# Kernel optimization log

Measured on AMD Instinct MI355X. Metric: run time of the kernel, lower is better.

## Reference

```python
import jax, jax.numpy as jnp
import numpy as np

B, H, T = 16, 2048, 512


def setup_inputs() -> dict:
    key = jax.random.key(0)
    ks = jax.random.split(key, 9)
    s = 1.0 / np.sqrt(H)
    return {
        "traj_z": jax.random.normal(ks[0], (B, H), dtype=jnp.float32),
        "traj_input": jax.random.normal(ks[1], (B, T), dtype=jnp.float32),
        "w_ih": jax.random.uniform(ks[2], (3 * H, 1), jnp.float32, -s, s),
        "b_ih": jax.random.uniform(ks[3], (3 * H,), jnp.float32, -s, s),
        "w_hh": jax.random.uniform(ks[4], (3 * H, H), jnp.float32, -s, s),
        "b_hh": jax.random.uniform(ks[5], (3 * H,), jnp.float32, -s, s),
        "w_traj": jax.random.uniform(ks[6], (1, H), jnp.float32, -s, s),
        "b_traj": jax.random.uniform(ks[7], (1,), jnp.float32, -s, s),
        "timesteps": T,
    }


def reference(traj_z, traj_input, w_ih, b_ih, w_hh, b_hh, w_traj, b_traj, timesteps):
    # epoch = inf -> teacher-forcing mask is all zeros -> blend is identity.
    x0 = traj_input[:, 0:1]  # [B, 1]

    def step(carry, _):
        h, x = carry
        gi = x @ w_ih.T + b_ih            # [B, 3H]
        gh = h @ w_hh.T + b_hh            # [B, 3H]
        i_r, i_z, i_n = jnp.split(gi, 3, axis=-1)
        h_r, h_z, h_n = jnp.split(gh, 3, axis=-1)
        r = jax.nn.sigmoid(i_r + h_r)
        z = jax.nn.sigmoid(i_z + h_z)
        n = jnp.tanh(i_n + r * h_n)
        h_new = (1.0 - z) * n + z * h     # GRUCell update
        x_new = h_new @ w_traj.T + b_traj + x  # residual linear head, [B, 1]
        return (h_new, x_new), x_new

    _, ys = jax.lax.scan(step, (traj_z, x0), None, length=timesteps)
    return jnp.transpose(ys, (1, 0, 2))  # [B, T, 1]
```

## Files before the change

kernel.cpp:

```cpp
#include <hip/hip_runtime.h>
#include <stdint.h>
#include <math.h>

#define Hdim   2048
#define Bdim   16
#define Tsteps 512
#define NWG    128
#define TPB    256
#define KC     16
#define NCHUNK 16
#define FLAGSTRIDE 32
#define HBYTES (Bdim * Hdim * 2)

typedef __attribute__((ext_vector_type(8))) short short8_t;
typedef __attribute__((ext_vector_type(4))) float f32x4;
typedef __attribute__((ext_vector_type(4))) unsigned int u32x4;

__device__ __forceinline__ short f2bf(float x) {
  uint32_t u = __builtin_bit_cast(uint32_t, x);
  u += 0x7fffu + ((u >> 16) & 1u);
  return (short)(u >> 16);
}

__device__ __forceinline__ short8_t load8_bf(const float* __restrict__ p) {
  short8_t r;
#pragma unroll
  for (int j = 0; j < 8; ++j) r[j] = f2bf(p[j]);
  return r;
}

__device__ __forceinline__ void publish(uint32_t* flags, int wg, int tid, uint32_t n) {
  asm volatile("s_waitcnt vmcnt(0)" ::: "memory");
  __syncthreads();
  if (tid == 0)
    __hip_atomic_store(flags + wg * FLAGSTRIDE, n, __ATOMIC_RELAXED, __HIP_MEMORY_SCOPE_AGENT);
}
__device__ __forceinline__ void waitall(const uint32_t* flags, int tid, uint32_t n) {
  if (tid < NWG) {
    while (__hip_atomic_load(flags + tid * FLAGSTRIDE, __ATOMIC_RELAXED,
                             __HIP_MEMORY_SCOPE_AGENT) < n) {
      __builtin_amdgcn_s_sleep(1);
    }
  }
  __syncthreads();
}


__device__ __forceinline__ void publish_h(uint32_t* hbuf32, int buf,
                                          int eb, int ekc, int ecol, float h_own) {
  uint32_t mybits = (uint32_t)(uint16_t)f2bf(h_own);
  uint32_t n1 = (uint32_t)__shfl_xor((int)mybits, 1, 64);
  uint32_t a  = (mybits & 0xffffu) | (n1 << 16);
  uint32_t b  = (uint32_t)__shfl_xor((int)a, 2, 64);
  uint32_t c4 = (uint32_t)__shfl_xor((int)a, 4, 64);
  uint32_t d  = (uint32_t)__shfl_xor((int)b, 4, 64);
  if ((ekc & 7) == 0) {
    u32x4 q; q.x = a; q.y = b; q.z = c4; q.w = d;
    char* dst = (char*)hbuf32 + (size_t)buf * HBYTES
              + ((size_t)(ecol >> 3) * 256 + (size_t)eb * 16);
    asm volatile("global_store_dwordx4 %0, %1, off sc0 sc1" :: "v"(dst), "v"(q) : "memory");
  }
}

__global__ void __launch_bounds__(TPB, 1) traj_kernel(
    const float* __restrict__ traj_z, const float* __restrict__ traj_input,
    const float* __restrict__ w_ih, const float* __restrict__ b_ih,
    const float* __restrict__ w_hh, const float* __restrict__ b_hh,
    const float* __restrict__ w_traj, const float* __restrict__ b_traj,
    float* __restrict__ out, uint32_t* __restrict__ hbuf32, uint32_t* __restrict__ flags)
{
  const int tid  = threadIdx.x;
  const int wg   = blockIdx.x;
  const int wave = tid >> 6;
  const int lane = tid & 63;
  const int ln16 = lane & 15;
  const int quad = lane >> 4;
  const int colbase = wg * KC;
  const int kwave   = wave * (Hdim / 4);

  __shared__ float s_red[4][3][16][16];
  __shared__ float s_x3[4][16];

  short8_t wf0[NCHUNK], wf1[NCHUNK], wf2[NCHUNK], wt[NCHUNK];
#pragma unroll
  for (int c = 0; c < NCHUNK; ++c) {
    const int k0 = kwave + c * 32 + quad * 8;
    wf0[c] = load8_bf(w_hh + (size_t)(0 * Hdim + colbase + ln16) * Hdim + k0);
    wf1[c] = load8_bf(w_hh + (size_t)(1 * Hdim + colbase + ln16) * Hdim + k0);
    wf2[c] = load8_bf(w_hh + (size_t)(2 * Hdim + colbase + ln16) * Hdim + k0);
    short8_t g = {0, 0, 0, 0, 0, 0, 0, 0};
    if (ln16 == 0) g = load8_bf(w_traj + k0);
    wt[c] = g;
  }

  const int eb   = tid >> 4;
  const int ekc  = tid & 15;
  const int ecol = colbase + ekc;
  const float wr = w_ih[ecol], wz = w_ih[Hdim + ecol], wn = w_ih[2 * Hdim + ecol];
  const float br = b_ih[ecol] + b_hh[ecol];
  const float bz = b_ih[Hdim + ecol] + b_hh[Hdim + ecol];
  const float bin = b_ih[2 * Hdim + ecol];
  const float bhn = b_hh[2 * Hdim + ecol];
  const float bt  = b_traj[0];
  float h_own = traj_z[eb * Hdim + ecol];
  float x_reg = traj_input[eb * Tsteps];

  publish_h(hbuf32, 0, eb, ekc, ecol, h_own);
  publish(flags, wg, tid, 1);

  for (int i = 0; i <= Tsteps; ++i) {
    waitall(flags, tid, (uint32_t)(i + 1));

    const char* hbase = (const char*)hbuf32 + (size_t)(i & 1) * HBYTES
                      + (size_t)(kwave >> 5) * 1024 + (size_t)lane * 16;
    short8_t af[NCHUNK];
#pragma unroll
    for (int c = 0; c < NCHUNK; ++c) {
      short8_t t;
      asm volatile("global_load_dwordx4 %0, %1, off sc0 sc1"
                   : "=v"(t) : "v"(hbase + (size_t)c * 1024));
      af[c] = t;
    }
    asm volatile("s_waitcnt vmcnt(0)" ::: "memory");
    __builtin_amdgcn_sched_barrier(0);

    f32x4 a0 = {0.f, 0.f, 0.f, 0.f}, a1 = a0, a2 = a0, a3 = a0;
#pragma unroll
    for (int c = 0; c < NCHUNK; ++c) {
      a0 = __builtin_amdgcn_mfma_f32_16x16x32_bf16(af[c], wf0[c], a0, 0, 0, 0);
      a1 = __builtin_amdgcn_mfma_f32_16x16x32_bf16(af[c], wf1[c], a1, 0, 0, 0);
      a2 = __builtin_amdgcn_mfma_f32_16x16x32_bf16(af[c], wf2[c], a2, 0, 0, 0);
      a3 = __builtin_amdgcn_mfma_f32_16x16x32_bf16(af[c], wt[c],  a3, 0, 0, 0);
    }

#pragma unroll
    for (int r = 0; r < 4; ++r) {
      const int m = quad * 4 + r;
      s_red[wave][0][m][ln16] = a0[r];
      s_red[wave][1][m][ln16] = a1[r];
      s_red[wave][2][m][ln16] = a2[r];
    }
    if (ln16 == 0) {
#pragma unroll
      for (int r = 0; r < 4; ++r) s_x3[wave][quad * 4 + r] = a3[r];
    }
    __syncthreads();

    if (i > 0) {
      const float xd = ((s_x3[0][eb] + s_x3[1][eb]) + s_x3[2][eb]) + s_x3[3][eb];
      x_reg += xd + bt;
      if (wg == 0 && ekc == 0) out[eb * Tsteps + (i - 1)] = x_reg;
    }
    if (i == Tsteps) break;

    const float gr = ((s_red[0][0][eb][ekc] + s_red[1][0][eb][ekc]) + s_red[2][0][eb][ekc]) + s_red[3][0][eb][ekc];
    const float gz = ((s_red[0][1][eb][ekc] + s_red[1][1][eb][ekc]) + s_red[2][1][eb][ekc]) + s_red[3][1][eb][ekc];
    const float gn = ((s_red[0][2][eb][ekc] + s_red[1][2][eb][ekc]) + s_red[2][2][eb][ekc]) + s_red[3][2][eb][ekc];
    const float x  = x_reg;
    const float rr = 1.f / (1.f + expf(-(x * wr + br + gr)));
    const float zz = 1.f / (1.f + expf(-(x * wz + bz + gz)));
    const float nn = tanhf(x * wn + bin + rr * (gn + bhn));
    h_own = (1.f - zz) * nn + zz * h_own;

    publish_h(hbuf32, (i + 1) & 1, eb, ekc, ecol, h_own);
    publish(flags, wg, tid, (uint32_t)(i + 2));
  }
}

extern "C" void kernel_launch(void* const* d_in, const int* in_sizes, int n_in,
                              void* d_out, int out_size, void* d_ws, size_t ws_size,
                              hipStream_t stream) {
  const float* traj_z     = (const float*)d_in[0];
  const float* traj_input = (const float*)d_in[1];
  const float* w_ih   = (const float*)d_in[2];
  const float* b_ih   = (const float*)d_in[3];
  const float* w_hh   = (const float*)d_in[4];
  const float* b_hh   = (const float*)d_in[5];
  const float* w_traj = (const float*)d_in[6];
  const float* b_traj = (const float*)d_in[7];
  float* out = (float*)d_out;

  uint8_t*  ws    = (uint8_t*)d_ws;
  uint32_t* flags = (uint32_t*)ws;
  uint32_t* hbuf  = (uint32_t*)(ws + NWG * FLAGSTRIDE * 4);

  (void)hipMemsetAsync(flags, 0, NWG * FLAGSTRIDE * 4, stream);
  hipLaunchKernelGGL(traj_kernel, dim3(NWG), dim3(TPB), 0, stream,
                     traj_z, traj_input, w_ih, b_ih, w_hh, b_hh, w_traj, b_traj,
                     out, hbuf, flags);
}
```

Measured before the change: 1.907 ms.

## Halve workgroup count with two column tiles each and publish partial head dots

The persistent kernel now runs 64 workgroups, each owning 32 hidden columns instead of 16. Five gate weight fragments stay in registers and the sixth (n gate, second tile) lives in LDS. The trajectory head is no longer an extra MFMA. Each workgroup publishes a partial dot product of its new h columns with w_traj, and every workgroup sums all 64 partials after the barrier. This is meant to halve the number of participants in the per-step grid barrier and drop the wasted head MFMA, at the cost of more MFMA and LDS work per workgroup and an extra global load per step.

```diff
diff --git a/kernel.cpp b/kernel.cpp
--- a/kernel.cpp
+++ b/kernel.cpp
@@ -5,9 +5,9 @@
 #define Hdim   2048
 #define Bdim   16
 #define Tsteps 512
-#define NWG    128
+#define NWG    64
 #define TPB    256
-#define KC     16
+#define KC     32
 #define NCHUNK 16
 #define FLAGSTRIDE 32
 #define HBYTES (Bdim * Hdim * 2)
@@ -44,7 +44,6 @@
   }
   __syncthreads();
 }
-
 
 __device__ __forceinline__ void publish_h(uint32_t* hbuf32, int buf,
                                           int eb, int ekc, int ecol, float h_own) {
@@ -62,12 +61,27 @@
   }
 }
 
+__device__ __forceinline__ void publish_part(float* partbuf, int buf, int wg,
+                                             int eb, int ekc,
+                                             float h0, float w0, float h1, float w1) {
+  float pd = h0 * w0 + h1 * w1;
+  pd += __shfl_xor(pd, 1, 64);
+  pd += __shfl_xor(pd, 2, 64);
+  pd += __shfl_xor(pd, 4, 64);
+  pd += __shfl_xor(pd, 8, 64);
+  if (ekc == 0) {
+    float* dst = partbuf + (size_t)buf * (Bdim * 64) + (size_t)eb * 64 + wg;
+    asm volatile("global_store_dword %0, %1, off sc0 sc1" :: "v"(dst), "v"(pd) : "memory");
+  }
+}
+
 __global__ void __launch_bounds__(TPB, 1) traj_kernel(
     const float* __restrict__ traj_z, const float* __restrict__ traj_input,
     const float* __restrict__ w_ih, const float* __restrict__ b_ih,
     const float* __restrict__ w_hh, const float* __restrict__ b_hh,
     const float* __restrict__ w_traj, const float* __restrict__ b_traj,
-    float* __restrict__ out, uint32_t* __restrict__ hbuf32, uint32_t* __restrict__ flags)
+    float* __restrict__ out, uint32_t* __restrict__ hbuf32,
+    float* __restrict__ partbuf, uint32_t* __restrict__ flags)
 {
   const int tid  = threadIdx.x;
   const int wg   = blockIdx.x;
@@ -77,35 +91,52 @@
   const int quad = lane >> 4;
   const int colbase = wg * KC;
   const int kwave   = wave * (Hdim / 4);
-
-  __shared__ float s_red[4][3][16][16];
-  __shared__ float s_x3[4][16];
-
-  short8_t wf0[NCHUNK], wf1[NCHUNK], wf2[NCHUNK], wt[NCHUNK];
+  const int gcbase  = wave * NCHUNK;
+
+  __shared__ short8_t s_wn1[64][64];
+  __shared__ float s_red[4][3][2][16][16];
+
+  for (int idx = tid; idx < 64 * 64; idx += TPB) {
+    const int gc = idx >> 6, l = idx & 63;
+    const int col = colbase + 16 + (l & 15);
+    const int k0  = gc * 32 + (l >> 4) * 8;
+    s_wn1[gc][l] = load8_bf(w_hh + (size_t)(2 * Hdim + col) * Hdim + k0);
+  }
+
+  short8_t fr0[NCHUNK], fz0[NCHUNK], fn0[NCHUNK], fr1[NCHUNK], fz1[NCHUNK];
 #pragma unroll
   for (int c = 0; c < NCHUNK; ++c) {
     const int k0 = kwave + c * 32 + quad * 8;
-    wf0[c] = load8_bf(w_hh + (size_t)(0 * Hdim + colbase + ln16) * Hdim + k0);
-    wf1[c] = load8_bf(w_hh + (size_t)(1 * Hdim + colbase + ln16) * Hdim + k0);
-    wf2[c] = load8_bf(w_hh + (size_t)(2 * Hdim + colbase + ln16) * Hdim + k0);
-    short8_t g = {0, 0, 0, 0, 0, 0, 0, 0};
-    if (ln16 == 0) g = load8_bf(w_traj + k0);
-    wt[c] = g;
+    fr0[c] = load8_bf(w_hh + (size_t)(0 * Hdim + colbase + ln16) * Hdim + k0);
+    fz0[c] = load8_bf(w_hh + (size_t)(1 * Hdim + colbase + ln16) * Hdim + k0);
+    fn0[c] = load8_bf(w_hh + (size_t)(2 * Hdim + colbase + ln16) * Hdim + k0);
+    fr1[c] = load8_bf(w_hh + (size_t)(0 * Hdim + colbase + 16 + ln16) * Hdim + k0);
+    fz1[c] = load8_bf(w_hh + (size_t)(1 * Hdim + colbase + 16 + ln16) * Hdim + k0);
   }
 
   const int eb   = tid >> 4;
   const int ekc  = tid & 15;
-  const int ecol = colbase + ekc;
-  const float wr = w_ih[ecol], wz = w_ih[Hdim + ecol], wn = w_ih[2 * Hdim + ecol];
-  const float br = b_ih[ecol] + b_hh[ecol];
-  const float bz = b_ih[Hdim + ecol] + b_hh[Hdim + ecol];
-  const float bin = b_ih[2 * Hdim + ecol];
-  const float bhn = b_hh[2 * Hdim + ecol];
-  const float bt  = b_traj[0];
-  float h_own = traj_z[eb * Hdim + ecol];
-  float x_reg = traj_input[eb * Tsteps];
-
-  publish_h(hbuf32, 0, eb, ekc, ecol, h_own);
+  const int col0 = colbase + ekc;
+  const int col1 = col0 + 16;
+  const float wr_0 = w_ih[col0], wz_0 = w_ih[Hdim + col0], wn_0 = w_ih[2 * Hdim + col0];
+  const float wr_1 = w_ih[col1], wz_1 = w_ih[Hdim + col1], wn_1 = w_ih[2 * Hdim + col1];
+  const float br_0 = b_ih[col0] + b_hh[col0];
+  const float bz_0 = b_ih[Hdim + col0] + b_hh[Hdim + col0];
+  const float bin_0 = b_ih[2 * Hdim + col0];
+  const float bhn_0 = b_hh[2 * Hdim + col0];
+  const float br_1 = b_ih[col1] + b_hh[col1];
+  const float bz_1 = b_ih[Hdim + col1] + b_hh[Hdim + col1];
+  const float bin_1 = b_ih[2 * Hdim + col1];
+  const float bhn_1 = b_hh[2 * Hdim + col1];
+  const float bt   = b_traj[0];
+  const float wtr0 = w_traj[col0], wtr1 = w_traj[col1];
+  float h_own0 = traj_z[eb * Hdim + col0];
+  float h_own1 = traj_z[eb * Hdim + col1];
+  float x_reg  = traj_input[eb * Tsteps];
+
+  publish_h(hbuf32, 0, eb, ekc, col0, h_own0);
+  publish_h(hbuf32, 0, eb, ekc, col1, h_own1);
+  publish_part(partbuf, 0, wg, eb, ekc, h_own0, wtr0, h_own1, wtr1);
   publish(flags, wg, tid, 1);
 
   for (int i = 0; i <= Tsteps; ++i) {
@@ -121,48 +152,70 @@
                    : "=v"(t) : "v"(hbase + (size_t)c * 1024));
       af[c] = t;
     }
+    f32x4 pdot;
+    {
+      const char* pbase = (const char*)partbuf + (size_t)(i & 1) * (Bdim * 64 * 4)
+                        + (size_t)eb * 256 + (size_t)ekc * 16;
+      asm volatile("global_load_dwordx4 %0, %1, off sc0 sc1"
+                   : "=v"(pdot) : "v"(pbase));
+    }
     asm volatile("s_waitcnt vmcnt(0)" ::: "memory");
     __builtin_amdgcn_sched_barrier(0);
 
-    f32x4 a0 = {0.f, 0.f, 0.f, 0.f}, a1 = a0, a2 = a0, a3 = a0;
+    f32x4 ar0 = {0.f, 0.f, 0.f, 0.f}, az0 = ar0, an0 = ar0;
+    f32x4 ar1 = ar0, az1 = ar0, an1 = ar0;
 #pragma unroll
     for (int c = 0; c < NCHUNK; ++c) {
-      a0 = __builtin_amdgcn_mfma_f32_16x16x32_bf16(af[c], wf0[c], a0, 0, 0, 0);
-      a1 = __builtin_amdgcn_mfma_f32_16x16x32_bf16(af[c], wf1[c], a1, 0, 0, 0);
-      a2 = __builtin_amdgcn_mfma_f32_16x16x32_bf16(af[c], wf2[c], a2, 0, 0, 0);
-      a3 = __builtin_amdgcn_mfma_f32_16x16x32_bf16(af[c], wt[c],  a3, 0, 0, 0);
+      const short8_t wn1f = s_wn1[gcbase + c][lane];
+      ar0 = __builtin_amdgcn_mfma_f32_16x16x32_bf16(af[c], fr0[c], ar0, 0, 0, 0);
+      az0 = __builtin_amdgcn_mfma_f32_16x16x32_bf16(af[c], fz0[c], az0, 0, 0, 0);
+      an0 = __builtin_amdgcn_mfma_f32_16x16x32_bf16(af[c], fn0[c], an0, 0, 0, 0);
+      ar1 = __builtin_amdgcn_mfma_f32_16x16x32_bf16(af[c], fr1[c], ar1, 0, 0, 0);
+      az1 = __builtin_amdgcn_mfma_f32_16x16x32_bf16(af[c], fz1[c], az1, 0, 0, 0);
+      an1 = __builtin_amdgcn_mfma_f32_16x16x32_bf16(af[c], wn1f,  an1, 0, 0, 0);
     }
 
 #pragma unroll
     for (int r = 0; r < 4; ++r) {
       const int m = quad * 4 + r;
-      s_red[wave][0][m][ln16] = a0[r];
-      s_red[wave][1][m][ln16] = a1[r];
-      s_red[wave][2][m][ln16] = a2[r];
-    }
-    if (ln16 == 0) {
-#pragma unroll
-      for (int r = 0; r < 4; ++r) s_x3[wave][quad * 4 + r] = a3[r];
+      s_red[wave][0][0][m][ln16] = ar0[r]; s_red[wave][0][1][m][ln16] = ar1[r];
+      s_red[wave][1][0][m][ln16] = az0[r]; s_red[wave][1][1][m][ln16] = az1[r];
+      s_red[wave][2][0][m][ln16] = an0[r]; s_red[wave][2][1][m][ln16] = an1[r];
     }
     __syncthreads();
 
     if (i > 0) {
-      const float xd = ((s_x3[0][eb] + s_x3[1][eb]) + s_x3[2][eb]) + s_x3[3][eb];
-      x_reg += xd + bt;
+      float S = (pdot[0] + pdot[1]) + (pdot[2] + pdot[3]);
+      S += __shfl_xor(S, 1, 64);
+      S += __shfl_xor(S, 2, 64);
+      S += __shfl_xor(S, 4, 64);
+      S += __shfl_xor(S, 8, 64);
+      x_reg += S + bt;
       if (wg == 0 && ekc == 0) out[eb * Tsteps + (i - 1)] = x_reg;
     }
     if (i == Tsteps) break;
 
-    const float gr = ((s_red[0][0][eb][ekc] + s_red[1][0][eb][ekc]) + s_red[2][0][eb][ekc]) + s_red[3][0][eb][ekc];
-    const float gz = ((s_red[0][1][eb][ekc] + s_red[1][1][eb][ekc]) + s_red[2][1][eb][ekc]) + s_red[3][1][eb][ekc];
-    const float gn = ((s_red[0][2][eb][ekc] + s_red[1][2][eb][ekc]) + s_red[2][2][eb][ekc]) + s_red[3][2][eb][ekc];
-    const float x  = x_reg;
-    const float rr = 1.f / (1.f + expf(-(x * wr + br + gr)));
-    const float zz = 1.f / (1.f + expf(-(x * wz + bz + gz)));
-    const float nn = tanhf(x * wn + bin + rr * (gn + bhn));
-    h_own = (1.f - zz) * nn + zz * h_own;
-
-    publish_h(hbuf32, (i + 1) & 1, eb, ekc, ecol, h_own);
+    const float x = x_reg;
+    const float gr_0 = ((s_red[0][0][0][eb][ekc] + s_red[1][0][0][eb][ekc]) + s_red[2][0][0][eb][ekc]) + s_red[3][0][0][eb][ekc];
+    const float gz_0 = ((s_red[0][1][0][eb][ekc] + s_red[1][1][0][eb][ekc]) + s_red[2][1][0][eb][ekc]) + s_red[3][1][0][eb][ekc];
+    const float gn_0 = ((s_red[0][2][0][eb][ekc] + s_red[1][2][0][eb][ekc]) + s_red[2][2][0][eb][ekc]) + s_red[3][2][0][eb][ekc];
+    const float gr_1 = ((s_red[0][0][1][eb][ekc] + s_red[1][0][1][eb][ekc]) + s_red[2][0][1][eb][ekc]) + s_red[3][0][1][eb][ekc];
+    const float gz_1 = ((s_red[0][1][1][eb][ekc] + s_red[1][1][1][eb][ekc]) + s_red[2][1][1][eb][ekc]) + s_red[3][1][1][eb][ekc];
+    const float gn_1 = ((s_red[0][2][1][eb][ekc] + s_red[1][2][1][eb][ekc]) + s_red[2][2][1][eb][ekc]) + s_red[3][2][1][eb][ekc];
+
+    const float rr0 = 1.f / (1.f + expf(-(x * wr_0 + br_0 + gr_0)));
+    const float zz0 = 1.f / (1.f + expf(-(x * wz_0 + bz_0 + gz_0)));
+    const float nn0 = tanhf(x * wn_0 + bin_0 + rr0 * (gn_0 + bhn_0));
+    h_own0 = (1.f - zz0) * nn0 + zz0 * h_own0;
+
+    const float rr1 = 1.f / (1.f + expf(-(x * wr_1 + br_1 + gr_1)));
+    const float zz1 = 1.f / (1.f + expf(-(x * wz_1 + bz_1 + gz_1)));
+    const float nn1 = tanhf(x * wn_1 + bin_1 + rr1 * (gn_1 + bhn_1));
+    h_own1 = (1.f - zz1) * nn1 + zz1 * h_own1;
+
+    publish_h(hbuf32, (i + 1) & 1, eb, ekc, col0, h_own0);
+    publish_h(hbuf32, (i + 1) & 1, eb, ekc, col1, h_own1);
+    publish_part(partbuf, (i + 1) & 1, wg, eb, ekc, h_own0, wtr0, h_own1, wtr1);
     publish(flags, wg, tid, (uint32_t)(i + 2));
   }
 }
@@ -182,10 +235,11 @@
 
   uint8_t*  ws    = (uint8_t*)d_ws;
   uint32_t* flags = (uint32_t*)ws;
-  uint32_t* hbuf  = (uint32_t*)(ws + NWG * FLAGSTRIDE * 4);
+  uint32_t* hbuf  = (uint32_t*)(ws + 16384);
+  float*    partb = (float*)(ws + 16384 + 2 * HBYTES);
 
   (void)hipMemsetAsync(flags, 0, NWG * FLAGSTRIDE * 4, stream);
   hipLaunchKernelGGL(traj_kernel, dim3(NWG), dim3(TPB), 0, stream,
                      traj_z, traj_input, w_ih, b_ih, w_hh, b_hh, w_traj, b_traj,
-                     out, hbuf, flags);
-}
+                     out, hbuf, partb, flags);
+}
```

New measurement: 2.651 ms. 39.0% more time.

## Per-wave wait on producer quarter and pipeline h loads with grouped MFMAs

Applied to the files above, without the earlier changes.

Each wave now spins only on the 32 flags of the workgroups whose hidden-state slice it reads, and no longer joins a block-wide barrier before loading. The 16 h-chunk loads are issued together and consumed in four groups with staged vmcnt waits, so MFMAs on early chunks overlap the later loads. This cuts the barrier and load-latency cost on the per-step critical path. The risk lies in memory ordering: it relies on relaxed flag loads followed by sc0 sc1 loads with no acquire fence, and on each wave reading only data from the workgroups it checked.

```diff
diff --git a/kernel.cpp b/kernel.cpp
--- a/kernel.cpp
+++ b/kernel.cpp
@@ -35,16 +35,16 @@
   if (tid == 0)
     __hip_atomic_store(flags + wg * FLAGSTRIDE, n, __ATOMIC_RELAXED, __HIP_MEMORY_SCOPE_AGENT);
 }
-__device__ __forceinline__ void waitall(const uint32_t* flags, int tid, uint32_t n) {
-  if (tid < NWG) {
-    while (__hip_atomic_load(flags + tid * FLAGSTRIDE, __ATOMIC_RELAXED,
-                             __HIP_MEMORY_SCOPE_AGENT) < n) {
+
+__device__ __forceinline__ void wait_quarter(const uint32_t* flags, int wave, int lane, uint32_t n) {
+  if (lane < 32) {
+    const uint32_t* f = flags + (wave * 32 + lane) * FLAGSTRIDE;
+    while (__hip_atomic_load(f, __ATOMIC_RELAXED, __HIP_MEMORY_SCOPE_AGENT) < n) {
       __builtin_amdgcn_s_sleep(1);
     }
   }
-  __syncthreads();
+  __builtin_amdgcn_sched_barrier(0);
 }
-
 
 __device__ __forceinline__ void publish_h(uint32_t* hbuf32, int buf,
                                           int eb, int ekc, int ecol, float h_own) {
@@ -109,29 +109,37 @@
   publish(flags, wg, tid, 1);
 
   for (int i = 0; i <= Tsteps; ++i) {
-    waitall(flags, tid, (uint32_t)(i + 1));
+    wait_quarter(flags, wave, lane, (uint32_t)(i + 1));
+
+    asm volatile("s_waitcnt vmcnt(0)" ::: "memory");
 
     const char* hbase = (const char*)hbuf32 + (size_t)(i & 1) * HBYTES
                       + (size_t)(kwave >> 5) * 1024 + (size_t)lane * 16;
     short8_t af[NCHUNK];
 #pragma unroll
     for (int c = 0; c < NCHUNK; ++c) {
-      short8_t t;
       asm volatile("global_load_dwordx4 %0, %1, off sc0 sc1"
-                   : "=v"(t) : "v"(hbase + (size_t)c * 1024));
-      af[c] = t;
+                   : "=v"(af[c]) : "v"(hbase + (size_t)c * 1024));
     }
-    asm volatile("s_waitcnt vmcnt(0)" ::: "memory");
-    __builtin_amdgcn_sched_barrier(0);
 
     f32x4 a0 = {0.f, 0.f, 0.f, 0.f}, a1 = a0, a2 = a0, a3 = a0;
-#pragma unroll
-    for (int c = 0; c < NCHUNK; ++c) {
-      a0 = __builtin_amdgcn_mfma_f32_16x16x32_bf16(af[c], wf0[c], a0, 0, 0, 0);
-      a1 = __builtin_amdgcn_mfma_f32_16x16x32_bf16(af[c], wf1[c], a1, 0, 0, 0);
-      a2 = __builtin_amdgcn_mfma_f32_16x16x32_bf16(af[c], wf2[c], a2, 0, 0, 0);
-      a3 = __builtin_amdgcn_mfma_f32_16x16x32_bf16(af[c], wt[c],  a3, 0, 0, 0);
+
+#define MFMA_GROUP(G, VM)                                                      \
+    asm volatile("s_waitcnt vmcnt(" #VM ")" ::: "memory");                     \
+    __builtin_amdgcn_sched_barrier(0);                                         \
+    _Pragma("unroll")                                                          \
+    for (int c = (G) * 4; c < (G) * 4 + 4; ++c) {                              \
+      a0 = __builtin_amdgcn_mfma_f32_16x16x32_bf16(af[c], wf0[c], a0, 0, 0, 0);\
+      a1 = __builtin_amdgcn_mfma_f32_16x16x32_bf16(af[c], wf1[c], a1, 0, 0, 0);\
+      a2 = __builtin_amdgcn_mfma_f32_16x16x32_bf16(af[c], wf2[c], a2, 0, 0, 0);\
+      a3 = __builtin_amdgcn_mfma_f32_16x16x32_bf16(af[c], wt[c],  a3, 0, 0, 0);\
     }
+
+    MFMA_GROUP(0, 12)
+    MFMA_GROUP(1, 8)
+    MFMA_GROUP(2, 4)
+    MFMA_GROUP(3, 0)
+#undef MFMA_GROUP
 
 #pragma unroll
     for (int r = 0; r < 4; ++r) {
```

Result: faster. 1.681 ms (-11.9%).

## Halve workgroup count, split grid barrier per wave, pipeline h loads with MFMAs

Applied to the files above, without the earlier changes.

Workgroups now own 32 hidden columns with 8 waves each, halving the number of participants in the per-step grid barrier. Each wave polls only the flags of the producers whose h chunks it reads, instead of a full-workgroup wait. Global h loads are consumed with staged vmcnt waits so the MFMAs overlap outstanding loads, and part of the n-gate weights lives in LDS to limit register pressure. The output store is moved after the publish. Costs are more register pressure and an 8-way LDS reduction.

```diff
diff --git a/kernel.cpp b/kernel.cpp
--- a/kernel.cpp
+++ b/kernel.cpp
@@ -5,10 +5,10 @@
 #define Hdim   2048
 #define Bdim   16
 #define Tsteps 512
-#define NWG    128
-#define TPB    256
-#define KC     16
-#define NCHUNK 16
+#define NWG    64
+#define TPB    512
+#define KC     32
+#define NCHUNK 8
 #define FLAGSTRIDE 32
 #define HBYTES (Bdim * Hdim * 2)
 
@@ -35,16 +35,16 @@
   if (tid == 0)
     __hip_atomic_store(flags + wg * FLAGSTRIDE, n, __ATOMIC_RELAXED, __HIP_MEMORY_SCOPE_AGENT);
 }
-__device__ __forceinline__ void waitall(const uint32_t* flags, int tid, uint32_t n) {
-  if (tid < NWG) {
-    while (__hip_atomic_load(flags + tid * FLAGSTRIDE, __ATOMIC_RELAXED,
-                             __HIP_MEMORY_SCOPE_AGENT) < n) {
+
+__device__ __forceinline__ void wait_eighth(const uint32_t* flags, int wave, int lane, uint32_t n) {
+  if (lane < 8) {
+    const uint32_t* f = flags + (wave * 8 + lane) * FLAGSTRIDE;
+    while (__hip_atomic_load(f, __ATOMIC_RELAXED, __HIP_MEMORY_SCOPE_AGENT) < n) {
       __builtin_amdgcn_s_sleep(1);
     }
   }
-  __syncthreads();
-}
-
+  __builtin_amdgcn_sched_barrier(0);
+}
 
 __device__ __forceinline__ void publish_h(uint32_t* hbuf32, int buf,
                                           int eb, int ekc, int ecol, float h_own) {
@@ -76,29 +76,40 @@
   const int ln16 = lane & 15;
   const int quad = lane >> 4;
   const int colbase = wg * KC;
-  const int kwave   = wave * (Hdim / 4);
-
-  __shared__ float s_red[4][3][16][16];
-  __shared__ float s_x3[4][16];
-
-  short8_t wf0[NCHUNK], wf1[NCHUNK], wf2[NCHUNK], wt[NCHUNK];
+  const int kwave   = wave * (Hdim / 8);
+  const int gcbase  = wave * NCHUNK;
+
+  __shared__ short8_t s_wn1[64][64];
+  __shared__ float s_red[8][3][2][16][16];
+  __shared__ float s_x3[8][16];
+
+  for (int idx = tid; idx < 64 * 64; idx += TPB) {
+    const int gc = idx >> 6, l = idx & 63;
+    const int col = colbase + 16 + (l & 15);
+    const int k0  = gc * 32 + (l >> 4) * 8;
+    s_wn1[gc][l] = load8_bf(w_hh + (size_t)(2 * Hdim + col) * Hdim + k0);
+  }
+
+  short8_t fr0[NCHUNK], fz0[NCHUNK], fn0[NCHUNK], fr1[NCHUNK], fz1[NCHUNK], wt[NCHUNK];
 #pragma unroll
   for (int c = 0; c < NCHUNK; ++c) {
     const int k0 = kwave + c * 32 + quad * 8;
-    wf0[c] = load8_bf(w_hh + (size_t)(0 * Hdim + colbase + ln16) * Hdim + k0);
-    wf1[c] = load8_bf(w_hh + (size_t)(1 * Hdim + colbase + ln16) * Hdim + k0);
-    wf2[c] = load8_bf(w_hh + (size_t)(2 * Hdim + colbase + ln16) * Hdim + k0);
+    fr0[c] = load8_bf(w_hh + (size_t)(0 * Hdim + colbase + ln16) * Hdim + k0);
+    fz0[c] = load8_bf(w_hh + (size_t)(1 * Hdim + colbase + ln16) * Hdim + k0);
+    fn0[c] = load8_bf(w_hh + (size_t)(2 * Hdim + colbase + ln16) * Hdim + k0);
+    fr1[c] = load8_bf(w_hh + (size_t)(0 * Hdim + colbase + 16 + ln16) * Hdim + k0);
+    fz1[c] = load8_bf(w_hh + (size_t)(1 * Hdim + colbase + 16 + ln16) * Hdim + k0);
     short8_t g = {0, 0, 0, 0, 0, 0, 0, 0};
     if (ln16 == 0) g = load8_bf(w_traj + k0);
     wt[c] = g;
   }
 
-  const int eb   = tid >> 4;
-  const int ekc  = tid & 15;
+  const int eb   = tid >> 5;
+  const int ekc  = tid & 31;
   const int ecol = colbase + ekc;
-  const float wr = w_ih[ecol], wz = w_ih[Hdim + ecol], wn = w_ih[2 * Hdim + ecol];
-  const float br = b_ih[ecol] + b_hh[ecol];
-  const float bz = b_ih[Hdim + ecol] + b_hh[Hdim + ecol];
+  const float wih_r = w_ih[ecol], wih_z = w_ih[Hdim + ecol], wih_n = w_ih[2 * Hdim + ecol];
+  const float br  = b_ih[ecol] + b_hh[ecol];
+  const float bz  = b_ih[Hdim + ecol] + b_hh[Hdim + ecol];
   const float bin = b_ih[2 * Hdim + ecol];
   const float bhn = b_hh[2 * Hdim + ecol];
   const float bt  = b_traj[0];
@@ -109,36 +120,57 @@
   publish(flags, wg, tid, 1);
 
   for (int i = 0; i <= Tsteps; ++i) {
-    waitall(flags, tid, (uint32_t)(i + 1));
+    wait_eighth(flags, wave, lane, (uint32_t)(i + 1));
+
+    asm volatile("s_waitcnt vmcnt(0)" ::: "memory");
 
     const char* hbase = (const char*)hbuf32 + (size_t)(i & 1) * HBYTES
                       + (size_t)(kwave >> 5) * 1024 + (size_t)lane * 16;
     short8_t af[NCHUNK];
 #pragma unroll
     for (int c = 0; c < NCHUNK; ++c) {
-      short8_t t;
       asm volatile("global_load_dwordx4 %0, %1, off sc0 sc1"
-                   : "=v"(t) : "v"(hbase + (size_t)c * 1024));
-      af[c] = t;
-    }
+                   : "=v"(af[c]) : "v"(hbase + (size_t)c * 1024));
+    }
+
+    f32x4 ar0 = {0.f, 0.f, 0.f, 0.f}, az0 = ar0, an0 = ar0;
+    f32x4 ar1 = ar0, az1 = ar0, an1 = ar0, a3 = ar0;
+
+    short8_t wnA = s_wn1[gcbase + 0][lane];
+    short8_t wnB = s_wn1[gcbase + 1][lane];
+
+#define CHAIN(c, wn)                                                            \
+    ar0 = __builtin_amdgcn_mfma_f32_16x16x32_bf16(af[c], fr0[c], ar0, 0, 0, 0); \
+    az0 = __builtin_amdgcn_mfma_f32_16x16x32_bf16(af[c], fz0[c], az0, 0, 0, 0); \
+    an0 = __builtin_amdgcn_mfma_f32_16x16x32_bf16(af[c], fn0[c], an0, 0, 0, 0); \
+    ar1 = __builtin_amdgcn_mfma_f32_16x16x32_bf16(af[c], fr1[c], ar1, 0, 0, 0); \
+    az1 = __builtin_amdgcn_mfma_f32_16x16x32_bf16(af[c], fz1[c], az1, 0, 0, 0); \
+    an1 = __builtin_amdgcn_mfma_f32_16x16x32_bf16(af[c], (wn),  an1, 0, 0, 0);  \
+    a3  = __builtin_amdgcn_mfma_f32_16x16x32_bf16(af[c], wt[c], a3,  0, 0, 0);
+
+    asm volatile("s_waitcnt vmcnt(6)" ::: "memory");
+    __builtin_amdgcn_sched_barrier(0);
+    CHAIN(0, wnA) CHAIN(1, wnB)
+    wnA = s_wn1[gcbase + 2][lane]; wnB = s_wn1[gcbase + 3][lane];
+    asm volatile("s_waitcnt vmcnt(4)" ::: "memory");
+    __builtin_amdgcn_sched_barrier(0);
+    CHAIN(2, wnA) CHAIN(3, wnB)
+    wnA = s_wn1[gcbase + 4][lane]; wnB = s_wn1[gcbase + 5][lane];
+    asm volatile("s_waitcnt vmcnt(2)" ::: "memory");
+    __builtin_amdgcn_sched_barrier(0);
+    CHAIN(4, wnA) CHAIN(5, wnB)
+    wnA = s_wn1[gcbase + 6][lane]; wnB = s_wn1[gcbase + 7][lane];
     asm volatile("s_waitcnt vmcnt(0)" ::: "memory");
     __builtin_amdgcn_sched_barrier(0);
-
-    f32x4 a0 = {0.f, 0.f, 0.f, 0.f}, a1 = a0, a2 = a0, a3 = a0;
-#pragma unroll
-    for (int c = 0; c < NCHUNK; ++c) {
-      a0 = __builtin_amdgcn_mfma_f32_16x16x32_bf16(af[c], wf0[c], a0, 0, 0, 0);
-      a1 = __builtin_amdgcn_mfma_f32_16x16x32_bf16(af[c], wf1[c], a1, 0, 0, 0);
-      a2 = __builtin_amdgcn_mfma_f32_16x16x32_bf16(af[c], wf2[c], a2, 0, 0, 0);
-      a3 = __builtin_amdgcn_mfma_f32_16x16x32_bf16(af[c], wt[c],  a3, 0, 0, 0);
-    }
+    CHAIN(6, wnA) CHAIN(7, wnB)
+#undef CHAIN
 
 #pragma unroll
     for (int r = 0; r < 4; ++r) {
       const int m = quad * 4 + r;
-      s_red[wave][0][m][ln16] = a0[r];
-      s_red[wave][1][m][ln16] = a1[r];
-      s_red[wave][2][m][ln16] = a2[r];
+      s_red[wave][0][0][m][ln16] = ar0[r]; s_red[wave][0][1][m][ln16] = ar1[r];
+      s_red[wave][1][0][m][ln16] = az0[r]; s_red[wave][1][1][m][ln16] = az1[r];
+      s_red[wave][2][0][m][ln16] = an0[r]; s_red[wave][2][1][m][ln16] = an1[r];
     }
     if (ln16 == 0) {
 #pragma unroll
@@ -147,23 +179,34 @@
     __syncthreads();
 
     if (i > 0) {
-      const float xd = ((s_x3[0][eb] + s_x3[1][eb]) + s_x3[2][eb]) + s_x3[3][eb];
+      float xd = s_x3[0][eb];
+#pragma unroll
+      for (int w = 1; w < 8; ++w) xd += s_x3[w][eb];
       x_reg += xd + bt;
+    }
+
+    if (i == Tsteps) {
       if (wg == 0 && ekc == 0) out[eb * Tsteps + (i - 1)] = x_reg;
-    }
-    if (i == Tsteps) break;
-
-    const float gr = ((s_red[0][0][eb][ekc] + s_red[1][0][eb][ekc]) + s_red[2][0][eb][ekc]) + s_red[3][0][eb][ekc];
-    const float gz = ((s_red[0][1][eb][ekc] + s_red[1][1][eb][ekc]) + s_red[2][1][eb][ekc]) + s_red[3][1][eb][ekc];
-    const float gn = ((s_red[0][2][eb][ekc] + s_red[1][2][eb][ekc]) + s_red[2][2][eb][ekc]) + s_red[3][2][eb][ekc];
+      break;
+    }
+
+    const int tt = ekc >> 4, nn_ = ekc & 15;
+    const float gr = ((s_red[0][0][tt][eb][nn_] + s_red[1][0][tt][eb][nn_]) + (s_red[2][0][tt][eb][nn_] + s_red[3][0][tt][eb][nn_]))
+                   + ((s_red[4][0][tt][eb][nn_] + s_red[5][0][tt][eb][nn_]) + (s_red[6][0][tt][eb][nn_] + s_red[7][0][tt][eb][nn_]));
+    const float gz = ((s_red[0][1][tt][eb][nn_] + s_red[1][1][tt][eb][nn_]) + (s_red[2][1][tt][eb][nn_] + s_red[3][1][tt][eb][nn_]))
+                   + ((s_red[4][1][tt][eb][nn_] + s_red[5][1][tt][eb][nn_]) + (s_red[6][1][tt][eb][nn_] + s_red[7][1][tt][eb][nn_]));
+    const float gn = ((s_red[0][2][tt][eb][nn_] + s_red[1][2][tt][eb][nn_]) + (s_red[2][2][tt][eb][nn_] + s_red[3][2][tt][eb][nn_]))
+                   + ((s_red[4][2][tt][eb][nn_] + s_red[5][2][tt][eb][nn_]) + (s_red[6][2][tt][eb][nn_] + s_red[7][2][tt][eb][nn_]));
+
     const float x  = x_reg;
-    const float rr = 1.f / (1.f + expf(-(x * wr + br + gr)));
-    const float zz = 1.f / (1.f + expf(-(x * wz + bz + gz)));
-    const float nn = tanhf(x * wn + bin + rr * (gn + bhn));
-    h_own = (1.f - zz) * nn + zz * h_own;
+    const float rr = 1.f / (1.f + expf(-(x * wih_r + br + gr)));
+    const float zz = 1.f / (1.f + expf(-(x * wih_z + bz + gz)));
+    const float nv = tanhf(x * wih_n + bin + rr * (gn + bhn));
+    h_own = (1.f - zz) * nv + zz * h_own;
 
     publish_h(hbuf32, (i + 1) & 1, eb, ekc, ecol, h_own);
     publish(flags, wg, tid, (uint32_t)(i + 2));
+    if (wg == 0 && i > 0 && ekc == 0) out[eb * Tsteps + (i - 1)] = x_reg;
   }
 }
 
@@ -182,7 +225,7 @@
 
   uint8_t*  ws    = (uint8_t*)d_ws;
   uint32_t* flags = (uint32_t*)ws;
-  uint32_t* hbuf  = (uint32_t*)(ws + NWG * FLAGSTRIDE * 4);
+  uint32_t* hbuf  = (uint32_t*)(ws + 16384);
 
   (void)hipMemsetAsync(flags, 0, NWG * FLAGSTRIDE * 4, stream);
   hipLaunchKernelGGL(traj_kernel, dim3(NWG), dim3(TPB), 0, stream,
```

Result: slower. 2.618 ms (+37.3%).
